# Kernel optimization log

Hardware: AMD Instinct MI355X
Metric: run time of the kernel (lower is better)

## Reference

```python
import jax, jax.numpy as jnp
import numpy as np

B, S, D, F, E = 8, 2048, 768, 3072, 8


def setup_inputs() -> dict:
    key = jax.random.key(0)
    k1, k2, k3, k4 = jax.random.split(key, 4)
    return {
        "hidden_states": jax.random.normal(k1, (B, S, D), dtype=jnp.float32),
        "router_w": jax.random.normal(k2, (D, E), dtype=jnp.float32) * 0.02,
        "w_in": jax.random.normal(k3, (E, D, F), dtype=jnp.float32) * 0.02,
        "w_out": jax.random.normal(k4, (E, F, D), dtype=jnp.float32) * 0.02,
    }


def reference(hidden_states, router_w, w_in, w_out):
    b, s, d = hidden_states.shape
    x = hidden_states.reshape(-1, d)                    # [T, D] tokens
    router_logits = x @ router_w                        # [T, E]
    router_probs_full = jax.nn.softmax(router_logits, axis=-1)
    expert_index = jnp.argmax(router_probs_full, axis=-1)          # top-1 routing
    onehot = jax.nn.one_hot(expert_index, E, dtype=x.dtype)        # [T, E] router_mask
    top_prob = jnp.max(router_probs_full, axis=-1, keepdims=True)  # [T, 1] router_probs

    # Per-expert FFN (relu MLP); every token is processed by exactly one expert,
    # expert outputs overwrite the token (gather/scatter combine in the original).
    y = jnp.zeros_like(x)
    for e in range(E):  # fixed small expert count; weights structurally distinct
        h = jax.nn.relu(x @ w_in[e]) @ w_out[e]
        y = y + onehot[:, e:e + 1] * h

    out = (top_prob * y).reshape(b, s, d)
    return out, router_logits, expert_index
```

## Files before the change

kernel.cpp:

```cpp
#include <hip/hip_runtime.h>
#include <hip/hip_bf16.h>

constexpr int T  = 16384;
constexpr int Dh = 768;
constexpr int Fh = 3072;
constexpr int Eh = 8;
constexpr int MAXTILES = 136;

typedef unsigned short ushort_t;
typedef __attribute__((ext_vector_type(8))) short  bf16x8;
typedef __attribute__((ext_vector_type(4))) float  f32x4;

static __device__ __forceinline__ ushort_t f2bf(float f) {
    unsigned u = __builtin_bit_cast(unsigned, f);
    u += 0x7FFFu + ((u >> 16) & 1u);
    return (ushort_t)(u >> 16);
}

__global__ void init_counts(int* counts) {
    if (threadIdx.x < Eh) counts[threadIdx.x] = 0;
}

__global__ __launch_bounds__(1024) void router_kernel(
    const float* __restrict__ x, const float* __restrict__ rw,
    float* __restrict__ logits_out, float* __restrict__ eidx_out,
    float* __restrict__ topp, int* __restrict__ counts, int* __restrict__ perm) {

    __shared__ float rwT[Eh][Dh];
    __shared__ int   sAmax[16];
    __shared__ int   sBase[Eh];

    int tid = threadIdx.x;
    for (int i = tid; i < Dh * Eh; i += 1024) {
        int d = i >> 3, e = i & 7;
        rwT[e][d] = rw[i];
    }
    __syncthreads();

    int wave = tid >> 6, lane = tid & 63;
    int t = blockIdx.x * 16 + wave;
    const float* xr = x + (size_t)t * Dh;

    double acc[Eh];
#pragma unroll
    for (int e = 0; e < Eh; ++e) acc[e] = 0.0;

#pragma unroll
    for (int j = 0; j < Dh / 256; ++j) {
        int d = lane * 4 + j * 256;
        const float4 xv = *(const float4*)(xr + d);
#pragma unroll
        for (int e = 0; e < Eh; ++e) {
            const float4 w = *(const float4*)&rwT[e][d];
            acc[e] += (double)xv.x * (double)w.x + (double)xv.y * (double)w.y
                    + (double)xv.z * (double)w.z + (double)xv.w * (double)w.w;
        }
    }
#pragma unroll
    for (int off = 32; off > 0; off >>= 1) {
#pragma unroll
        for (int e = 0; e < Eh; ++e) acc[e] += __shfl_xor(acc[e], off, 64);
    }

    int amax = 0;
    if (lane == 0) {
        float l32[Eh];
        float m = -3.4e38f;
#pragma unroll
        for (int e = 0; e < Eh; ++e) l32[e] = (float)acc[e];
#pragma unroll
        for (int e = 0; e < Eh; ++e) {
            if (l32[e] > m) { m = l32[e]; amax = e; }
        }
        float s = 0.f;
#pragma unroll
        for (int e = 0; e < Eh; ++e) s += expf(l32[e] - m);
#pragma unroll
        for (int e = 0; e < Eh; ++e) logits_out[(size_t)t * Eh + e] = l32[e];
        eidx_out[t] = (float)amax;
        topp[t]     = 1.0f / s;
        sAmax[wave] = amax;
    }
    __syncthreads();

    if (tid < Eh) {
        int c = 0;
#pragma unroll
        for (int w = 0; w < 16; ++w) c += (sAmax[w] == tid);
        sBase[tid] = (c > 0) ? atomicAdd(&counts[tid], c) : 0;
    }
    __syncthreads();

    if (lane == 0) {
        int prior = 0;
        for (int w = 0; w < wave; ++w) prior += (sAmax[w] == amax);
        perm[amax * T + sBase[amax] + prior] = t;
    }
}

__global__ void scan_counts(const int* counts, int* offsets,
                            int* tE, int* tGoff, int* tSlot0, int* tRows, int* nT) {
    if (threadIdx.x == 0) {
        int off = 0, n = 0;
        for (int e = 0; e < Eh; ++e) {
            offsets[e] = off;
            int c = counts[e];
            for (int t0 = 0; t0 < c; t0 += 128) {
                tE[n] = e; tGoff[n] = off + t0; tSlot0[n] = t0;
                tRows[n] = (c - t0 < 128) ? (c - t0) : 128;
                ++n;
            }
            off += c;
        }
        offsets[Eh] = off;
        nT[0] = n;
    }
}

__global__ void gather_cast_x(const float* __restrict__ x, const int* __restrict__ offsets,
                              const int* __restrict__ perm, ushort_t* __restrict__ Xg) {
    __shared__ int soff[Eh + 1];
    if (threadIdx.x < Eh + 1) soff[threadIdx.x] = offsets[threadIdx.x];
    __syncthreads();
    int q  = blockIdx.x * 256 + threadIdx.x;
    int g  = q / (Dh / 4);
    int cq = (q - g * (Dh / 4)) * 4;
    int e = 0;
#pragma unroll
    for (int i = 1; i < Eh; ++i) e += (g >= soff[i]);
    int tok = perm[e * T + (g - soff[e])];
    const float4 v = *(const float4*)(x + (size_t)tok * Dh + cq);
    ushort4 o;
    o.x = f2bf(v.x); o.y = f2bf(v.y); o.z = f2bf(v.z); o.w = f2bf(v.w);
    *(ushort4*)(Xg + (size_t)g * Dh + cq) = o;
}

__global__ void transpose_cvt(const float* __restrict__ src, ushort_t* __restrict__ dst,
                              int R, int C) {
    __shared__ ushort_t tile[32][33];
    int tx = threadIdx.x, ty = threadIdx.y;
    size_t base = (size_t)blockIdx.z * (size_t)R * (size_t)C;
    int c0 = blockIdx.x * 32, r0 = blockIdx.y * 32;
#pragma unroll
    for (int j = 0; j < 4; ++j) {
        int r = ty + j * 8;
        tile[r][tx] = f2bf(src[base + (size_t)(r0 + r) * C + c0 + tx]);
    }
    __syncthreads();
    int idx = ty * 32 + tx;
#pragma unroll
    for (int j = 0; j < 2; ++j) {
        int lin = idx + j * 256;
        int c  = lin >> 4;
        int rp = (lin & 15) * 2;
        ushort2 o = { tile[rp][c], tile[rp + 1][c] };
        *(ushort2*)(dst + base + (size_t)(c0 + c) * R + r0 + rp) = o;
    }
}

template<int KTOT, int NTOT, int MODE>
__global__ __launch_bounds__(256) void moe_gemm(
    const ushort_t* __restrict__ Aall, const ushort_t* __restrict__ Ball,
    const int* __restrict__ tE, const int* __restrict__ tGoff,
    const int* __restrict__ tSlot0, const int* __restrict__ tRows,
    const int* __restrict__ nT,
    const int* __restrict__ perm, const float* __restrict__ topp,
    void* __restrict__ Cout)
{
    int i = blockIdx.x;
    if (i >= nT[0]) return;
    int e     = tE[i];
    int goff  = tGoff[i];
    int slot0 = tSlot0[i];
    int rows  = tRows[i];
    int n0    = blockIdx.y * 128;

    const ushort_t* Ap = Aall + (size_t)goff * KTOT;
    const ushort_t* Bp = Ball + (size_t)e * KTOT * NTOT + (size_t)n0 * KTOT;

    __shared__ ushort_t As[128 * 64];
    __shared__ ushort_t Bs[128 * 64];
    __shared__ int   tokLds[128];
    __shared__ float probLds[128];

    int tid = threadIdx.x, lane = tid & 63, wave = tid >> 6;

    if (MODE == 1 && tid < 128) {
        int tok = (tid < rows) ? perm[e * T + slot0 + tid] : 0;
        tokLds[tid]  = tok;
        probLds[tid] = (tid < rows) ? topp[tok] : 0.f;
    }

    f32x4 acc[4][4];
    const f32x4 zero = {0.f, 0.f, 0.f, 0.f};
#pragma unroll
    for (int mi = 0; mi < 4; ++mi)
#pragma unroll
        for (int ni = 0; ni < 4; ++ni) acc[mi][ni] = zero;

    int lrow  = lane >> 3;
    int gsrc8 = ((lane & 7) ^ lrow) * 8;
    int wm    = (wave >> 1) * 64;
    int wn    = (wave & 1) * 64;
    int lm    = lane & 15;
    int lm7   = lm & 7;
    int gq    = lane >> 4;

    for (int k0 = 0; k0 < KTOT; k0 += 64) {
#pragma unroll
        for (int it = 0; it < 4; ++it) {
            int rb  = wave * 4 + it;
            int row = rb * 8 + lrow;
            const ushort_t* ga = Ap + (size_t)row * KTOT + k0 + gsrc8;
            const ushort_t* gb = Bp + (size_t)row * KTOT + k0 + gsrc8;
            __builtin_amdgcn_global_load_lds(
                (const __attribute__((address_space(1))) unsigned int*)ga,
                (__attribute__((address_space(3))) unsigned int*)&As[rb * 512], 16, 0, 0);
            __builtin_amdgcn_global_load_lds(
                (const __attribute__((address_space(1))) unsigned int*)gb,
                (__attribute__((address_space(3))) unsigned int*)&Bs[rb * 512], 16, 0, 0);
        }
        __syncthreads();
#pragma unroll
        for (int kc = 0; kc < 64; kc += 32) {
            int cbase = gq + (kc >> 3);
            bf16x8 af[4], bb[4];
#pragma unroll
            for (int mi = 0; mi < 4; ++mi) {
                int row = wm + mi * 16 + lm;
                af[mi] = *(const bf16x8*)&As[row * 64 + ((cbase ^ lm7) * 8)];
            }
#pragma unroll
            for (int ni = 0; ni < 4; ++ni) {
                int row = wn + ni * 16 + lm;
                bb[ni] = *(const bf16x8*)&Bs[row * 64 + ((cbase ^ lm7) * 8)];
            }
#pragma unroll
            for (int mi = 0; mi < 4; ++mi)
#pragma unroll
                for (int ni = 0; ni < 4; ++ni)
                    acc[mi][ni] = __builtin_amdgcn_mfma_f32_16x16x32_bf16(
                        af[mi], bb[ni], acc[mi][ni], 0, 0, 0);
        }
        __syncthreads();
    }

    int cr = (lane >> 4) * 4;
    int cc = lane & 15;
#pragma unroll
    for (int mi = 0; mi < 4; ++mi) {
#pragma unroll
        for (int r = 0; r < 4; ++r) {
            int m = wm + mi * 16 + cr + r;
            if (m < rows) {
                if (MODE == 0) {
                    ushort_t* hp = (ushort_t*)Cout + (size_t)(goff + m) * NTOT + n0 + wn + cc;
#pragma unroll
                    for (int ni = 0; ni < 4; ++ni) {
                        float v = acc[mi][ni][r];
                        hp[ni * 16] = f2bf(v > 0.f ? v : 0.f);
                    }
                } else {
                    int tok = tokLds[m];
                    float p = probLds[m];
                    float* op = (float*)Cout + (size_t)tok * NTOT + n0 + wn + cc;
#pragma unroll
                    for (int ni = 0; ni < 4; ++ni) op[ni * 16] = acc[mi][ni][r] * p;
                }
            }
        }
    }
}

constexpr size_t OFF_COUNTS  = 0;
constexpr size_t OFF_OFFSETS = 256;
constexpr size_t OFF_TILES   = 512;
constexpr size_t OFF_TOPP    = OFF_TILES + 4 * 144 * 5 + 64;
constexpr size_t OFF_PERM    = OFF_TOPP + (size_t)T * 4;
constexpr size_t OFF_XG      = (OFF_PERM + (size_t)Eh * T * 4 + 255) & ~(size_t)255;
constexpr size_t OFF_H       = (OFF_XG + (size_t)(T + 128) * Dh * 2 + 255) & ~(size_t)255;
constexpr size_t OFF_WIN     = (OFF_H + (size_t)(T + 128) * Fh * 2 + 255) & ~(size_t)255;
constexpr size_t OFF_WOUT    = (OFF_WIN + (size_t)Eh * Dh * Fh * 2 + 255) & ~(size_t)255;

extern "C" void kernel_launch(void* const* d_in, const int* in_sizes, int n_in,
                              void* d_out, int out_size, void* d_ws, size_t ws_size,
                              hipStream_t stream) {
    const float* x    = (const float*)d_in[0];
    const float* rw   = (const float*)d_in[1];
    const float* w_in = (const float*)d_in[2];
    const float* w_out= (const float*)d_in[3];

    float* out    = (float*)d_out;
    float* logits = out + (size_t)T * Dh;
    float* eidx   = logits + (size_t)T * Eh;

    char* ws = (char*)d_ws;
    int*      counts  = (int*)(ws + OFF_COUNTS);
    int*      offsets = (int*)(ws + OFF_OFFSETS);
    int*      tE      = (int*)(ws + OFF_TILES);
    int*      tGoff   = tE + 144;
    int*      tSlot0  = tGoff + 144;
    int*      tRows   = tSlot0 + 144;
    int*      nT      = tRows + 144;
    float*    topp    = (float*)(ws + OFF_TOPP);
    int*      perm    = (int*)(ws + OFF_PERM);
    ushort_t* Xg      = (ushort_t*)(ws + OFF_XG);
    ushort_t* h       = (ushort_t*)(ws + OFF_H);
    ushort_t* WinT    = (ushort_t*)(ws + OFF_WIN);
    ushort_t* WoutT   = (ushort_t*)(ws + OFF_WOUT);

    init_counts<<<1, 64, 0, stream>>>(counts);
    router_kernel<<<T / 16, 1024, 0, stream>>>(x, rw, logits, eidx, topp, counts, perm);
    scan_counts<<<1, 64, 0, stream>>>(counts, offsets, tE, tGoff, tSlot0, tRows, nT);
    gather_cast_x<<<(T * (Dh / 4)) / 256, 256, 0, stream>>>(x, offsets, perm, Xg);
    transpose_cvt<<<dim3(Fh / 32, Dh / 32, Eh), dim3(32, 8), 0, stream>>>(w_in, WinT, Dh, Fh);
    transpose_cvt<<<dim3(Dh / 32, Fh / 32, Eh), dim3(32, 8), 0, stream>>>(w_out, WoutT, Fh, Dh);
    moe_gemm<Dh, Fh, 0><<<dim3(MAXTILES, Fh / 128), 256, 0, stream>>>(
        Xg, WinT, tE, tGoff, tSlot0, tRows, nT, perm, topp, (void*)h);
    moe_gemm<Fh, Dh, 1><<<dim3(MAXTILES, Dh / 128), 256, 0, stream>>>(
        h, WoutT, tE, tGoff, tSlot0, tRows, nT, perm, topp, (void*)out);
}
```

Before: 547.9 us.

## Rewrite MoE GEMM as 256x256 tile with double-buffered LDS prefetch pipeline

Replaces the 128x128, 256-thread MoE GEMM with a 256x256 tile, 512-thread kernel whose LDS is double-buffered. Next-k-tile global-to-LDS loads are interleaved with four quadrant MFMA phases using explicit vmcnt waits, barriers and setprio. Tiles per expert are regrouped into chunks of 256 rows, and partial tiles clamp their source rows. The aim is more data reuse per block and hidden load latency, at the cost of more LDS (about 128KB), higher register pressure, fewer blocks and more padding waste on partial expert tiles.

```diff
diff --git a/kernel.cpp b/kernel.cpp
--- a/kernel.cpp
+++ b/kernel.cpp
@@ -5,7 +5,7 @@
 constexpr int Dh = 768;
 constexpr int Fh = 3072;
 constexpr int Eh = 8;
-constexpr int MAXTILES = 136;
+constexpr int MAXT2 = T / 256 + Eh;
 
 typedef unsigned short ushort_t;
 typedef __attribute__((ext_vector_type(8))) short  bf16x8;
@@ -105,9 +105,9 @@
         for (int e = 0; e < Eh; ++e) {
             offsets[e] = off;
             int c = counts[e];
-            for (int t0 = 0; t0 < c; t0 += 128) {
+            for (int t0 = 0; t0 < c; t0 += 256) {
                 tE[n] = e; tGoff[n] = off + t0; tSlot0[n] = t0;
-                tRows[n] = (c - t0 < 128) ? (c - t0) : 128;
+                tRows[n] = (c - t0 < 256) ? (c - t0) : 256;
                 ++n;
             }
             off += c;
@@ -159,7 +159,7 @@
 }
 
 template<int KTOT, int NTOT, int MODE>
-__global__ __launch_bounds__(256) void moe_gemm(
+__global__ __launch_bounds__(512, 2) void moe_gemm2(
     const ushort_t* __restrict__ Aall, const ushort_t* __restrict__ Ball,
     const int* __restrict__ tE, const int* __restrict__ tGoff,
     const int* __restrict__ tSlot0, const int* __restrict__ tRows,
@@ -173,103 +173,174 @@
     int goff  = tGoff[i];
     int slot0 = tSlot0[i];
     int rows  = tRows[i];
-    int n0    = blockIdx.y * 128;
+    int n0    = blockIdx.y * 256;
 
     const ushort_t* Ap = Aall + (size_t)goff * KTOT;
     const ushort_t* Bp = Ball + (size_t)e * KTOT * NTOT + (size_t)n0 * KTOT;
 
-    __shared__ ushort_t As[128 * 64];
-    __shared__ ushort_t Bs[128 * 64];
-    __shared__ int   tokLds[128];
-    __shared__ float probLds[128];
-
-    int tid = threadIdx.x, lane = tid & 63, wave = tid >> 6;
-
-    if (MODE == 1 && tid < 128) {
+    __shared__ ushort_t As[2][256 * 64];
+    __shared__ ushort_t Bs[2][256 * 64];
+    __shared__ int   tokLds[256];
+    __shared__ float probLds[256];
+
+    int tid = threadIdx.x, lane = tid & 63, wid = tid >> 6;
+    int wr2 = wid >> 2, wc2 = wid & 3;
+    int gq  = lane >> 4, lm = lane & 15, l7 = lane & 7;
+
+    if (MODE == 1 && tid < 256) {
         int tok = (tid < rows) ? perm[e * T + slot0 + tid] : 0;
         tokLds[tid]  = tok;
         probLds[tid] = (tid < rows) ? topp[tok] : 0.f;
     }
 
-    f32x4 acc[4][4];
+    f32x4 acc[4][4][2];
     const f32x4 zero = {0.f, 0.f, 0.f, 0.f};
 #pragma unroll
-    for (int mi = 0; mi < 4; ++mi)
-#pragma unroll
-        for (int ni = 0; ni < 4; ++ni) acc[mi][ni] = zero;
-
-    int lrow  = lane >> 3;
-    int gsrc8 = ((lane & 7) ^ lrow) * 8;
-    int wm    = (wave >> 1) * 64;
-    int wn    = (wave & 1) * 64;
-    int lm    = lane & 15;
-    int lm7   = lm & 7;
-    int gq    = lane >> 4;
-
-    for (int k0 = 0; k0 < KTOT; k0 += 64) {
-#pragma unroll
-        for (int it = 0; it < 4; ++it) {
-            int rb  = wave * 4 + it;
-            int row = rb * 8 + lrow;
-            const ushort_t* ga = Ap + (size_t)row * KTOT + k0 + gsrc8;
-            const ushort_t* gb = Bp + (size_t)row * KTOT + k0 + gsrc8;
-            __builtin_amdgcn_global_load_lds(
-                (const __attribute__((address_space(1))) unsigned int*)ga,
-                (__attribute__((address_space(3))) unsigned int*)&As[rb * 512], 16, 0, 0);
-            __builtin_amdgcn_global_load_lds(
-                (const __attribute__((address_space(1))) unsigned int*)gb,
-                (__attribute__((address_space(3))) unsigned int*)&Bs[rb * 512], 16, 0, 0);
-        }
-        __syncthreads();
-#pragma unroll
-        for (int kc = 0; kc < 64; kc += 32) {
-            int cbase = gq + (kc >> 3);
-            bf16x8 af[4], bb[4];
-#pragma unroll
-            for (int mi = 0; mi < 4; ++mi) {
-                int row = wm + mi * 16 + lm;
-                af[mi] = *(const bf16x8*)&As[row * 64 + ((cbase ^ lm7) * 8)];
-            }
-#pragma unroll
-            for (int ni = 0; ni < 4; ++ni) {
-                int row = wn + ni * 16 + lm;
-                bb[ni] = *(const bf16x8*)&Bs[row * 64 + ((cbase ^ lm7) * 8)];
-            }
-#pragma unroll
-            for (int mi = 0; mi < 4; ++mi)
-#pragma unroll
-                for (int ni = 0; ni < 4; ++ni)
-                    acc[mi][ni] = __builtin_amdgcn_mfma_f32_16x16x32_bf16(
-                        af[mi], bb[ni], acc[mi][ni], 0, 0, 0);
-        }
-        __syncthreads();
+    for (int q = 0; q < 4; ++q)
+#pragma unroll
+        for (int mi = 0; mi < 4; ++mi)
+#pragma unroll
+            for (int ni = 0; ni < 2; ++ni) acc[q][mi][ni] = zero;
+
+    bf16x8 af[2][4];
+    bf16x8 bb[2][2];
+
+#define STAGE_A(BUF, HALF, KT) { \
+    _Pragma("unroll") \
+    for (int j = 0; j < 2; ++j) { \
+        int c_ = tid + j * 512; \
+        int rr = c_ >> 3, gg = c_ & 7; \
+        int row_ = (HALF) * 128 + rr; \
+        int srow_ = row_ < rows ? row_ : rows - 1; \
+        const ushort_t* src_ = Ap + (size_t)srow_ * KTOT + (size_t)(KT) * 64 + ((gg ^ (rr & 7)) << 3); \
+        __builtin_amdgcn_global_load_lds( \
+            (const __attribute__((address_space(1))) unsigned int*)src_, \
+            (__attribute__((address_space(3))) unsigned int*)&As[BUF][(size_t)row_ * 64 + gg * 8], 16, 0, 0); \
+    } }
+
+#define STAGE_B(BUF, HALF, KT) { \
+    _Pragma("unroll") \
+    for (int j = 0; j < 2; ++j) { \
+        int c_ = tid + j * 512; \
+        int rr = c_ >> 3, gg = c_ & 7; \
+        int row_ = (HALF) * 128 + rr; \
+        const ushort_t* src_ = Bp + (size_t)row_ * KTOT + (size_t)(KT) * 64 + ((gg ^ (rr & 7)) << 3); \
+        __builtin_amdgcn_global_load_lds( \
+            (const __attribute__((address_space(1))) unsigned int*)src_, \
+            (__attribute__((address_space(3))) unsigned int*)&Bs[BUF][(size_t)row_ * 64 + gg * 8], 16, 0, 0); \
+    } }
+
+#define READ_FRAGS(TB, AH, BH) { \
+    _Pragma("unroll") \
+    for (int ks = 0; ks < 2; ++ks) { \
+        const int cs_ = (((ks << 2) + gq) ^ l7) << 3; \
+        _Pragma("unroll") \
+        for (int mi = 0; mi < 4; ++mi) \
+            af[ks][mi] = *(const bf16x8*)&As[TB][((AH) * 128 + wr2 * 64 + mi * 16 + lm) * 64 + cs_]; \
+        _Pragma("unroll") \
+        for (int ni = 0; ni < 2; ++ni) \
+            bb[ks][ni] = *(const bf16x8*)&Bs[TB][((BH) * 128 + wc2 * 32 + ni * 16 + lm) * 64 + cs_]; \
+    } }
+
+#define MFMA_Q(Q) { \
+    __builtin_amdgcn_s_setprio(1); \
+    _Pragma("unroll") \
+    for (int ks = 0; ks < 2; ++ks) \
+        _Pragma("unroll") \
+        for (int mi = 0; mi < 4; ++mi) \
+            _Pragma("unroll") \
+            for (int ni = 0; ni < 2; ++ni) \
+                acc[Q][mi][ni] = __builtin_amdgcn_mfma_f32_16x16x32_bf16( \
+                    af[ks][mi], bb[ks][ni], acc[Q][mi][ni], 0, 0, 0); \
+    __builtin_amdgcn_s_setprio(0); }
+
+    const int nkt = KTOT / 64;
+
+    STAGE_A(0, 0, 0);
+    STAGE_A(0, 1, 0);
+    STAGE_B(0, 0, 0);
+    STAGE_B(0, 1, 0);
+    if (nkt > 1) {
+        STAGE_B(1, 0, 1);
+        STAGE_A(1, 0, 1);
+        asm volatile("s_waitcnt vmcnt(4)" ::: "memory");
+    } else {
+        asm volatile("s_waitcnt vmcnt(0)" ::: "memory");
+    }
+    __builtin_amdgcn_sched_barrier(0);
+    __builtin_amdgcn_s_barrier();
+
+    for (int t = 0; t < nkt; ++t) {
+        const int TB = t & 1;
+
+        READ_FRAGS(TB, 0, 0);
+        if (t + 1 < nkt) {
+            STAGE_A(TB ^ 1, 1, t + 1);
+            STAGE_B(TB ^ 1, 1, t + 1);
+        }
+        __builtin_amdgcn_s_barrier();
+        MFMA_Q(0);
+        __builtin_amdgcn_s_barrier();
+
+        READ_FRAGS(TB, 1, 0);
+        __builtin_amdgcn_s_barrier();
+        MFMA_Q(1);
+        __builtin_amdgcn_s_barrier();
+
+        READ_FRAGS(TB, 0, 1);
+        if (t + 2 < nkt) STAGE_B(TB, 0, t + 2);
+        __builtin_amdgcn_s_barrier();
+        MFMA_Q(2);
+        __builtin_amdgcn_s_barrier();
+
+        READ_FRAGS(TB, 1, 1);
+        if (t + 2 < nkt) {
+            STAGE_A(TB, 0, t + 2);
+            asm volatile("s_waitcnt vmcnt(4)" ::: "memory");
+        } else {
+            asm volatile("s_waitcnt vmcnt(0)" ::: "memory");
+        }
+        __builtin_amdgcn_sched_barrier(0);
+        __builtin_amdgcn_s_barrier();
+        MFMA_Q(3);
+        __builtin_amdgcn_s_barrier();
     }
 
     int cr = (lane >> 4) * 4;
     int cc = lane & 15;
 #pragma unroll
-    for (int mi = 0; mi < 4; ++mi) {
-#pragma unroll
-        for (int r = 0; r < 4; ++r) {
-            int m = wm + mi * 16 + cr + r;
-            if (m < rows) {
-                if (MODE == 0) {
-                    ushort_t* hp = (ushort_t*)Cout + (size_t)(goff + m) * NTOT + n0 + wn + cc;
-#pragma unroll
-                    for (int ni = 0; ni < 4; ++ni) {
-                        float v = acc[mi][ni][r];
-                        hp[ni * 16] = f2bf(v > 0.f ? v : 0.f);
+    for (int q = 0; q < 4; ++q) {
+        const int ah = q & 1, bh = q >> 1;
+#pragma unroll
+        for (int mi = 0; mi < 4; ++mi) {
+#pragma unroll
+            for (int r = 0; r < 4; ++r) {
+                int m = ah * 128 + wr2 * 64 + mi * 16 + cr + r;
+                if (m < rows) {
+                    if (MODE == 0) {
+                        ushort_t* hp = (ushort_t*)Cout + (size_t)(goff + m) * NTOT
+                                     + n0 + bh * 128 + wc2 * 32 + cc;
+#pragma unroll
+                        for (int ni = 0; ni < 2; ++ni) {
+                            float v = acc[q][mi][ni][r];
+                            hp[ni * 16] = f2bf(v > 0.f ? v : 0.f);
+                        }
+                    } else {
+                        int tok = tokLds[m];
+                        float p = probLds[m];
+                        float* op = (float*)Cout + (size_t)tok * NTOT
+                                  + n0 + bh * 128 + wc2 * 32 + cc;
+#pragma unroll
+                        for (int ni = 0; ni < 2; ++ni) op[ni * 16] = acc[q][mi][ni][r] * p;
                     }
-                } else {
-                    int tok = tokLds[m];
-                    float p = probLds[m];
-                    float* op = (float*)Cout + (size_t)tok * NTOT + n0 + wn + cc;
-#pragma unroll
-                    for (int ni = 0; ni < 4; ++ni) op[ni * 16] = acc[mi][ni][r] * p;
                 }
             }
         }
     }
+#undef STAGE_A
+#undef STAGE_B
+#undef READ_FRAGS
+#undef MFMA_Q
 }
 
 constexpr size_t OFF_COUNTS  = 0;
@@ -315,8 +386,8 @@
     gather_cast_x<<<(T * (Dh / 4)) / 256, 256, 0, stream>>>(x, offsets, perm, Xg);
     transpose_cvt<<<dim3(Fh / 32, Dh / 32, Eh), dim3(32, 8), 0, stream>>>(w_in, WinT, Dh, Fh);
     transpose_cvt<<<dim3(Dh / 32, Fh / 32, Eh), dim3(32, 8), 0, stream>>>(w_out, WoutT, Fh, Dh);
-    moe_gemm<Dh, Fh, 0><<<dim3(MAXTILES, Fh / 128), 256, 0, stream>>>(
+    moe_gemm2<Dh, Fh, 0><<<dim3(MAXT2, Fh / 256), 512, 0, stream>>>(
         Xg, WinT, tE, tGoff, tSlot0, tRows, nT, perm, topp, (void*)h);
-    moe_gemm<Fh, Dh, 1><<<dim3(MAXTILES, Dh / 128), 256, 0, stream>>>(
+    moe_gemm2<Fh, Dh, 1><<<dim3(MAXT2, Dh / 256), 512, 0, stream>>>(
         h, WoutT, tE, tGoff, tSlot0, tRows, nT, perm, topp, (void*)out);
 }
```

New measurement: 511.2 us. 6.7% less time.
